# Kernel tuning notes

Hardware: AMD Instinct MI355X
Metric: run time of the kernel (lower is better)

## Reference

```python
import jax, jax.numpy as jnp
import numpy as np

B, C_IN, H, W = 4, 8, 128, 128
C_OUT, KH, KW = 16, 5, 5


def _patches(img, kh, kw):
    """Extract valid sliding windows. img: [B,C,H,W] -> [B, C, kh*kw, Ho, Wo]."""
    b, c, h, w = img.shape
    ho, wo = h - kh + 1, w - kw + 1
    views = [img[:, :, i:i + ho, j:j + wo] for i in range(kh) for j in range(kw)]
    return jnp.stack(views, axis=2)  # small fixed loop over kh*kw offsets


def setup_inputs() -> dict:
    key = jax.random.key(0)
    k1, k2 = jax.random.split(key)
    img = jax.random.normal(k1, (B, C_IN, H, W), dtype=jnp.float32)
    kernel = jax.random.normal(k2, (C_OUT, C_IN, KH, KW), dtype=jnp.float32)
    return {"img": img, "kernel": kernel}


def reference(img, kernel):
    # Max-plus (tropical) semifield convolution, kind='conv':
    # out[b,o,y,x] = max_{c,i,j} ( img[b,c,y+i,x+j] + kernel_flipped[o,c,i,j] )
    kflip = kernel[:, :, ::-1, ::-1]            # true convolution: flip kernel spatially
    o, c, kh, kw = kflip.shape
    p = _patches(img, kh, kw)                    # [B, C, K, Ho, Wo], K = kh*kw
    b, _, k, ho, wo = p.shape
    p = p.reshape(b, c * k, ho * wo)             # [B, R, P]   R = C*K reduction dim
    wmat = kflip.reshape(o, c * k)               # [O, R]
    # tropical matmul: broadcast-add then max-reduce over R
    out = jnp.max(wmat[None, :, :, None] + p[:, None, :, :], axis=2)  # [B, O, P]
    return out.reshape(b, o, ho, wo)
```

## Files before the change

kernel.cpp:

```cpp
#include <hip/hip_runtime.h>
#include <math.h>

#define B_  4
#define CI  8
#define HH  128
#define WW  128
#define CO  16
#define KH  5
#define KW  5
#define HO  124
#define WO  124

#define TX  32
#define TY  8
#define THREADS 512

__global__ __launch_bounds__(THREADS, 4)
void maxplus_conv4(const float* __restrict__ img,
                   const float* __restrict__ kern,
                   float* __restrict__ out)
{
    __shared__ __align__(16) float ilds[CI][TY + KH - 1][TX + KW - 1];

    const int tid   = threadIdx.x;
    const int x0    = blockIdx.x * TX;
    const int y0    = blockIdx.y * TY;
    const int bz    = blockIdx.z;
    const int b     = bz >> 1;
    const int ohalf = bz & 1;

    const float* imgb = img + (size_t)b * CI * HH * WW;
    #pragma unroll
    for (int it = 0; it < 2; ++it) {
        const int idx = tid + it * THREADS;
        if (idx < 864) {
            const int c   = idx / 108;
            const int rem = idx - c * 108;
            const int r   = rem / 9;
            const int f4  = rem - r * 9;
            const int gy = y0 + r;
            const int gx = x0 + f4 * 4;
            float4 v;
            if (gy < HH && gx < WW) {
                v = *(const float4*)&imgb[(c * HH + gy) * WW + gx];
            } else {
                v.x = v.y = v.z = v.w = -INFINITY;
            }
            *(float4*)&ilds[c][r][f4 * 4] = v;
        }
    }
    __syncthreads();

    const int tx = tid & 7;
    const int ty = (tid >> 3) & 7;
    const int o = __builtin_amdgcn_readfirstlane(ohalf * 8 + (tid >> 6));

    const float* wp = kern + (size_t)o * (CI * KH * KW);

    float acc[4];
    #pragma unroll
    for (int p = 0; p < 4; ++p) acc[p] = -INFINITY;

    #pragma unroll 1
    for (int c = 0; c < CI; ++c) {
        float w[25];
        #pragma unroll
        for (int t = 0; t < 25; ++t) w[t] = wp[c * 25 + t];
        float4 va[5], vb[5];
        #pragma unroll
        for (int i = 0; i < KH; ++i) {
            const float* vp = &ilds[c][ty + i][tx * 4];
            va[i] = *(const float4*)vp;
            vb[i] = *(const float4*)(vp + 4);
        }
        #pragma unroll
        for (int i = 0; i < KH; ++i) {
            const float v[8] = {va[i].x, va[i].y, va[i].z, va[i].w,
                                vb[i].x, vb[i].y, vb[i].z, vb[i].w};
            #pragma unroll
            for (int p = 0; p < 4; ++p) {
                float T[5];
                #pragma unroll
                for (int j = 0; j < KW; ++j) {
                    const int wi = (4 - i) * KW + (4 - j);
                    T[j] = v[p + j] + w[wi];
                }
                const float m0 = fmaxf(fmaxf(acc[p], T[0]), T[1]);
                const float m1 = fmaxf(fmaxf(T[2], T[3]), T[4]);
                acc[p] = fmaxf(m0, m1);
            }
        }
    }

    const int y = y0 + ty;
    const int x = x0 + tx * 4;
    if (y < HO && x < WO) {
        float4 s;
        s.x = acc[0]; s.y = acc[1]; s.z = acc[2]; s.w = acc[3];
        *(float4*)&out[(((size_t)b * CO + o) * HO + y) * WO + x] = s;
    }
}

extern "C" void kernel_launch(void* const* d_in, const int* in_sizes, int n_in,
                              void* d_out, int out_size, void* d_ws, size_t ws_size,
                              hipStream_t stream)
{
    const float* img  = (const float*)d_in[0];
    const float* kern = (const float*)d_in[1];
    float* out = (float*)d_out;

    dim3 grid((WO + TX - 1) / TX, (HO + TY - 1) / TY, B_ * 2);
    dim3 block(THREADS);
    maxplus_conv4<<<grid, block, 0, stream>>>(img, kern, out);
}
```

Before: 15.09 us.

## Compute two output channels per thread with packed f32x2 adds and double-buffered prefetch

After: 18.59 us. 1.23x slower.

```diff
diff --git a/kernel.cpp b/kernel.cpp
--- a/kernel.cpp
+++ b/kernel.cpp
@@ -13,10 +13,12 @@
 
 #define TX  32
 #define TY  8
-#define THREADS 512
+#define THREADS 256
 
-__global__ __launch_bounds__(THREADS, 4)
-void maxplus_conv4(const float* __restrict__ img,
+using f32x2 = __attribute__((ext_vector_type(2))) float;
+
+__global__ __launch_bounds__(THREADS)
+void maxplus_conv6(const float* __restrict__ img,
                    const float* __restrict__ kern,
                    float* __restrict__ out)
 {
@@ -31,21 +33,17 @@
 
     const float* imgb = img + (size_t)b * CI * HH * WW;
     #pragma unroll
-    for (int it = 0; it < 2; ++it) {
+    for (int it = 0; it < 4; ++it) {
         const int idx = tid + it * THREADS;
         if (idx < 864) {
             const int c   = idx / 108;
             const int rem = idx - c * 108;
             const int r   = rem / 9;
             const int f4  = rem - r * 9;
-            const int gy = y0 + r;
-            const int gx = x0 + f4 * 4;
+            const int gy = y0 + r, gx = x0 + f4 * 4;
             float4 v;
-            if (gy < HH && gx < WW) {
-                v = *(const float4*)&imgb[(c * HH + gy) * WW + gx];
-            } else {
-                v.x = v.y = v.z = v.w = -INFINITY;
-            }
+            if (gy < HH && gx < WW) v = *(const float4*)&imgb[(c * HH + gy) * WW + gx];
+            else { v.x = v.y = v.z = v.w = -INFINITY; }
             *(float4*)&ilds[c][r][f4 * 4] = v;
         }
     }
@@ -53,51 +51,75 @@
 
     const int tx = tid & 7;
     const int ty = (tid >> 3) & 7;
-    const int o = __builtin_amdgcn_readfirstlane(ohalf * 8 + (tid >> 6));
+    const int o0 = __builtin_amdgcn_readfirstlane(ohalf * 8 + ((tid >> 6) << 1));
 
-    const float* wp = kern + (size_t)o * (CI * KH * KW);
+    const float* w0p = kern + (size_t)o0 * (CI * KH * KW);
+    const float* w1p = w0p + CI * KH * KW;
 
-    float acc[4];
+    float accx[4], accy[4];
     #pragma unroll
-    for (int p = 0; p < 4; ++p) acc[p] = -INFINITY;
+    for (int p = 0; p < 4; ++p) { accx[p] = -INFINITY; accy[p] = -INFINITY; }
 
+    float4 vaA[5], vbA[5], vaB[5], vbB[5];
+    f32x2 WA[25], WB[25];
+
+#define PREF_IMG(S, c) do { \
+    _Pragma("unroll") \
+    for (int i = 0; i < KH; ++i) { \
+        const float* vp = &ilds[c][ty + i][tx * 4]; \
+        va##S[i] = *(const float4*)vp; \
+        vb##S[i] = *(const float4*)(vp + 4); \
+    } } while (0)
+
+#define PREF_W(S, c) do { \
+    _Pragma("unroll") \
+    for (int t = 0; t < 25; ++t) { \
+        W##S[t].x = w0p[(c) * 25 + (24 - t)]; \
+        W##S[t].y = w1p[(c) * 25 + (24 - t)]; \
+    } } while (0)
+
+#define COMP(S) do { \
+    _Pragma("unroll") \
+    for (int i = 0; i < KH; ++i) { \
+        const float vv[8] = {va##S[i].x, va##S[i].y, va##S[i].z, va##S[i].w, \
+                             vb##S[i].x, vb##S[i].y, vb##S[i].z, vb##S[i].w}; \
+        _Pragma("unroll") \
+        for (int p = 0; p < 4; ++p) { \
+            f32x2 t0 = (f32x2){vv[p + 0], vv[p + 0]} + W##S[i * 5 + 0]; \
+            f32x2 t1 = (f32x2){vv[p + 1], vv[p + 1]} + W##S[i * 5 + 1]; \
+            f32x2 t2 = (f32x2){vv[p + 2], vv[p + 2]} + W##S[i * 5 + 2]; \
+            f32x2 t3 = (f32x2){vv[p + 3], vv[p + 3]} + W##S[i * 5 + 3]; \
+            f32x2 t4 = (f32x2){vv[p + 4], vv[p + 4]} + W##S[i * 5 + 4]; \
+            accx[p] = fmaxf(fmaxf(fmaxf(accx[p], t0.x), t1.x), \
+                            fmaxf(fmaxf(t2.x, t3.x), t4.x)); \
+            accy[p] = fmaxf(fmaxf(fmaxf(accy[p], t0.y), t1.y), \
+                            fmaxf(fmaxf(t2.y, t3.y), t4.y)); \
+        } \
+    } } while (0)
+
+    PREF_IMG(A, 0);
+    PREF_W(A, 0);
     #pragma unroll 1
-    for (int c = 0; c < CI; ++c) {
-        float w[25];
-        #pragma unroll
-        for (int t = 0; t < 25; ++t) w[t] = wp[c * 25 + t];
-        float4 va[5], vb[5];
-        #pragma unroll
-        for (int i = 0; i < KH; ++i) {
-            const float* vp = &ilds[c][ty + i][tx * 4];
-            va[i] = *(const float4*)vp;
-            vb[i] = *(const float4*)(vp + 4);
+    for (int cp = 0; cp < CI / 2; ++cp) {
+        const int c0 = cp * 2;
+        PREF_IMG(B, c0 + 1);
+        PREF_W(B, c0 + 1);
+        COMP(A);
+        if (cp < CI / 2 - 1) {
+            PREF_IMG(A, c0 + 2);
+            PREF_W(A, c0 + 2);
         }
-        #pragma unroll
-        for (int i = 0; i < KH; ++i) {
-            const float v[8] = {va[i].x, va[i].y, va[i].z, va[i].w,
-                                vb[i].x, vb[i].y, vb[i].z, vb[i].w};
-            #pragma unroll
-            for (int p = 0; p < 4; ++p) {
-                float T[5];
-                #pragma unroll
-                for (int j = 0; j < KW; ++j) {
-                    const int wi = (4 - i) * KW + (4 - j);
-                    T[j] = v[p + j] + w[wi];
-                }
-                const float m0 = fmaxf(fmaxf(acc[p], T[0]), T[1]);
-                const float m1 = fmaxf(fmaxf(T[2], T[3]), T[4]);
-                acc[p] = fmaxf(m0, m1);
-            }
-        }
+        COMP(B);
     }
 
     const int y = y0 + ty;
     const int x = x0 + tx * 4;
     if (y < HO && x < WO) {
-        float4 s;
-        s.x = acc[0]; s.y = acc[1]; s.z = acc[2]; s.w = acc[3];
-        *(float4*)&out[(((size_t)b * CO + o) * HO + y) * WO + x] = s;
+        float4 s0, s1;
+        s0.x = accx[0]; s0.y = accx[1]; s0.z = accx[2]; s0.w = accx[3];
+        s1.x = accy[0]; s1.y = accy[1]; s1.z = accy[2]; s1.w = accy[3];
+        *(float4*)&out[(((size_t)b * CO + o0) * HO + y) * WO + x] = s0;
+        *(float4*)&out[(((size_t)b * CO + o0 + 1) * HO + y) * WO + x] = s1;
     }
 }
 
@@ -111,5 +133,5 @@
 
     dim3 grid((WO + TX - 1) / TX, (HO + TY - 1) / TY, B_ * 2);
     dim3 block(THREADS);
-    maxplus_conv4<<<grid, block, 0, stream>>>(img, kern, out);
+    maxplus_conv6<<<grid, block, 0, stream>>>(img, kern, out);
 }
```
